# Performance work log

Hardware: AMD Instinct MI355X
Metric: run time of the kernel (lower is better)

## Reference

```python
import jax, jax.numpy as jnp
import numpy as np

NUM_HEADS = 12
HEAD_DIM = 128
DIM = NUM_HEADS * HEAD_DIM  # 1536
FRAMES = 8
GRID_H, GRID_W = 15, 26
SPATIAL = GRID_H * GRID_W  # 390
SEQ = FRAMES * SPATIAL      # 3120
EPS = 1e-5


def setup_inputs() -> dict:
    key = jax.random.key(0)
    ks = jax.random.split(key, 12)
    w = lambda k, shape, s=0.02: jax.random.normal(k, shape, dtype=jnp.float32) * s
    return {
        "x": jax.random.normal(ks[0], (1, SEQ, DIM), dtype=jnp.float32),
        "freqs": jax.random.uniform(ks[1], (SEQ, HEAD_DIM // 2), dtype=jnp.float32) * 6.283,
        "Wq": w(ks[2], (DIM, DIM)), "bq": jnp.zeros((DIM,), jnp.float32), "gq": jnp.ones((DIM,), jnp.float32),
        "Wk": w(ks[3], (DIM, DIM)), "bk": jnp.zeros((DIM,), jnp.float32), "gk": jnp.ones((DIM,), jnp.float32),
        "Wv": w(ks[4], (DIM, DIM)), "bv": jnp.zeros((DIM,), jnp.float32),
        "Wo": w(ks[5], (DIM, DIM)), "bo": jnp.zeros((DIM,), jnp.float32),
        "qk_frame_bias": w(ks[6], (FRAMES, DIM), 0.05),
        "v_frame_bias": w(ks[7], (FRAMES, DIM), 0.05),
        "v_spatial_bias": w(ks[8], (SPATIAL, DIM), 0.05),
    }


def _rmsnorm(x, g):
    return x * jax.lax.rsqrt(jnp.mean(x * x, axis=-1, keepdims=True) + EPS) * g


def _rope(x, freqs):
    # x: [b, s, dim] -> per-head interleaved complex rotation (Wan-style)
    b, s, _ = x.shape
    xp = x.reshape(b, s, NUM_HEADS, HEAD_DIM // 2, 2)
    cos = jnp.cos(freqs)[None, :, None, :]  # [1, s, 1, d/2]
    sin = jnp.sin(freqs)[None, :, None, :]
    xr, xi = xp[..., 0], xp[..., 1]
    out = jnp.stack([xr * cos - xi * sin, xr * sin + xi * cos], axis=-1)
    return out.reshape(b, s, DIM)


def _expand_frame(bias):
    # [FRAMES, dim] -> [1, FRAMES*SPATIAL, dim] (each frame vector repeated over spatial tokens)
    return jnp.broadcast_to(bias[:, None, :], (FRAMES, SPATIAL, DIM)).reshape(1, SEQ, DIM)


def _expand_spatial(bias):
    # [SPATIAL, dim] -> [1, FRAMES*SPATIAL, dim] (tiled over frames)
    return jnp.broadcast_to(bias[None, :, :], (FRAMES, SPATIAL, DIM)).reshape(1, SEQ, DIM)


def reference(x, freqs, Wq, bq, gq, Wk, bk, gk, Wv, bv, Wo, bo,
              qk_frame_bias, v_frame_bias, v_spatial_bias):
    q = _rmsnorm(x @ Wq + bq, gq)
    k = _rmsnorm(x @ Wk + bk, gk)
    v = x @ Wv + bv
    q = _rope(q, freqs)
    k = _rope(k, freqs)
    qk_bias = _expand_frame(qk_frame_bias)
    q = q + qk_bias
    k = k + qk_bias
    v = v + _expand_frame(v_frame_bias) + _expand_spatial(v_spatial_bias)
    b, s, _ = x.shape
    qh = q.reshape(b, s, NUM_HEADS, HEAD_DIM)
    kh = k.reshape(b, s, NUM_HEADS, HEAD_DIM)
    vh = v.reshape(b, s, NUM_HEADS, HEAD_DIM)
    scale = 1.0 / np.sqrt(HEAD_DIM)
    scores = jnp.einsum("bqnd,bknd->bnqk", qh, kh) * scale
    attn = jax.nn.softmax(scores, axis=-1)
    out = jnp.einsum("bnqk,bknd->bqnd", attn, vh).reshape(b, s, DIM)
    return out @ Wo + bo
```

## Files before the change

kernel.cpp:

```cpp
#include <hip/hip_runtime.h>
#include <cstdint>

#define SEQ     3120
#define SPAD    3200
#define DIM     1536
#define NQKV    4608
#define HEADS   12
#define HD      128
#define SPATIAL 390
#define EPSV    1e-5f
#define KVBLK   64
#define NTILES  49
#define NEGBIG  (-1e30f)
#define QSCALE  (0.08838834764831845f * 1.4426950408889634f)
#define CROW(r, hi) ((((r) & 3) + 8 * ((r) >> 2)) + 4 * (hi))

typedef unsigned short u16;
typedef short s16x8 __attribute__((ext_vector_type(8)));
typedef float f32x4 __attribute__((ext_vector_type(4)));
typedef float f32x16 __attribute__((ext_vector_type(16)));

__device__ __forceinline__ u16 f2bf(float f) {
  union { float f; unsigned u; } v; v.f = f;
  unsigned r = v.u + 0x7FFFu + ((v.u >> 16) & 1u);
  return (u16)(r >> 16);
}
__device__ __forceinline__ float bf2f(u16 b) {
  union { unsigned u; float f; } v; v.u = ((unsigned)b) << 16;
  return v.f;
}
__device__ __forceinline__ unsigned cvtpk(float lo, float hi) {
  unsigned r;
  asm("v_cvt_pk_bf16_f32 %0, %1, %2" : "=v"(r) : "v"(lo), "v"(hi));
  return r;
}
__device__ __forceinline__ void gload16(const void* g, const void* l) {
  __builtin_amdgcn_global_load_lds(
      (const __attribute__((address_space(1))) unsigned*)g,
      (__attribute__((address_space(3))) unsigned*)(uintptr_t)l,
      16, 0, 0);
}

__global__ __launch_bounds__(256) void k_convert_x(const float* __restrict__ x,
                                                   u16* __restrict__ xb) {
  const int i = (blockIdx.x * 256 + threadIdx.x) * 4;
  if (i >= SPAD * DIM) return;
  const int row = i / DIM;
  float4 v = make_float4(0.f, 0.f, 0.f, 0.f);
  if (row < SEQ) v = *(const float4*)(x + i);
  const unsigned lo = (unsigned)f2bf(v.x) | ((unsigned)f2bf(v.y) << 16);
  const unsigned hi = (unsigned)f2bf(v.z) | ((unsigned)f2bf(v.w) << 16);
  *(uint2*)(xb + i) = make_uint2(lo, hi);
}

__global__ __launch_bounds__(256) void k_transpose_w(
    const float* __restrict__ Wq, const float* __restrict__ Wk,
    const float* __restrict__ Wv, const float* __restrict__ Wo,
    u16* __restrict__ WtAll, u16* __restrict__ WoT) {
  const int wsel = blockIdx.z;
  const float* W = (wsel == 0) ? Wq : (wsel == 1) ? Wk : (wsel == 2) ? Wv : Wo;
  __shared__ float t[32][33];
  const int k0 = blockIdx.x * 32, n0 = blockIdx.y * 32;
  const int c = threadIdx.x & 31, r8 = threadIdx.x >> 5;
#pragma unroll
  for (int rr = 0; rr < 32; rr += 8)
    t[r8 + rr][c] = W[(size_t)(k0 + r8 + rr) * DIM + n0 + c];
  __syncthreads();
  u16* Wt = (wsel < 3) ? (WtAll + (size_t)wsel * DIM * DIM) : WoT;
#pragma unroll
  for (int rr = 0; rr < 32; rr += 8)
    Wt[(size_t)(n0 + r8 + rr) * DIM + k0 + c] = f2bf(t[c][r8 + rr]);
}

__global__ void k_biascat(const float* __restrict__ bq, const float* __restrict__ bk,
                          const float* __restrict__ bv, float* __restrict__ bcat) {
  const int i = blockIdx.x * 256 + threadIdx.x;
  if (i >= NQKV) return;
  bcat[i] = (i < DIM) ? bq[i] : (i < 2 * DIM) ? bk[i - DIM] : bv[i - 2 * DIM];
}

template <int OUT_BF16>
__global__ __launch_bounds__(256) void k_gemm(const u16* __restrict__ A,
                                              const u16* __restrict__ Bt,
                                              const float* __restrict__ bias,
                                              void* __restrict__ Cout,
                                              int N, int K, int storeMmax) {
  __shared__ short As[4096];
  __shared__ short Bs[4096];
  const int tid = threadIdx.x;
  const int lane = tid & 63, wv = tid >> 6;
  const int l15 = lane & 15, g = lane >> 4;
  const int brow = blockIdx.y * 128, bcol = blockIdx.x * 128;
  const int wr = wv >> 1, wc = wv & 1;

  const f32x4 z4 = {0.f, 0.f, 0.f, 0.f};
  f32x4 acc[4][4];
#pragma unroll
  for (int m = 0; m < 4; ++m)
#pragma unroll
    for (int n = 0; n < 4; ++n) acc[m][n] = z4;

  const int srow = wv * 16 + (lane >> 2);
  const int skk = (lane & 3) * 8;
  const u16* Ab = A + (size_t)(brow + srow) * K + skk;
  const u16* Bb = Bt + (size_t)(bcol + srow) * K + skk;
  short* AsW = As + wv * 512;
  short* BsW = Bs + wv * 512;
  const size_t step64 = (size_t)64 * K;

  for (int k0 = 0; k0 < K; k0 += 32) {
    __syncthreads();
    gload16(Ab + k0, AsW);
    gload16(Ab + k0 + step64, AsW + 2048);
    gload16(Bb + k0, BsW);
    gload16(Bb + k0 + step64, BsW + 2048);
    __syncthreads();
    s16x8 a[4], b[4];
#pragma unroll
    for (int m = 0; m < 4; ++m)
      a[m] = *(const s16x8*)&As[(wr * 64 + m * 16 + l15) * 32 + g * 8];
#pragma unroll
    for (int n = 0; n < 4; ++n)
      b[n] = *(const s16x8*)&Bs[(wc * 64 + n * 16 + l15) * 32 + g * 8];
#pragma unroll
    for (int m = 0; m < 4; ++m)
#pragma unroll
      for (int n = 0; n < 4; ++n)
        acc[m][n] = __builtin_amdgcn_mfma_f32_16x16x32_bf16(a[m], b[n], acc[m][n], 0, 0, 0);
  }

#pragma unroll
  for (int m = 0; m < 4; ++m) {
#pragma unroll
    for (int n = 0; n < 4; ++n) {
      const int cc = bcol + wc * 64 + n * 16 + l15;
      const float bb = bias[cc];
#pragma unroll
      for (int i = 0; i < 4; ++i) {
        const int r = brow + wr * 64 + m * 16 + g * 4 + i;
        if (r < storeMmax) {
          const float v = acc[m][n][i] + bb;
          if (OUT_BF16) ((u16*)Cout)[(size_t)r * N + cc] = f2bf(v);
          else          ((float*)Cout)[(size_t)r * N + cc] = v;
        }
      }
    }
  }
}

__global__ __launch_bounds__(256) void k_post(
    const u16* __restrict__ Pqkv, const float* __restrict__ freqs,
    const float* __restrict__ gq, const float* __restrict__ gk,
    const float* __restrict__ qkfb, const float* __restrict__ vfb,
    const float* __restrict__ vsb,
    u16* __restrict__ Qf, u16* __restrict__ Kf, u16* __restrict__ Vf) {
  const int s = blockIdx.x;
  const int t = threadIdx.x;
  const int fidx = s / SPATIAL;
  const int sp = s - fidx * SPATIAL;
  __shared__ float cs[64], sn[64];
  __shared__ float red[8];
  if (t < 64) {
    const float a = freqs[s * 64 + t];
    cs[t] = __cosf(a);
    sn[t] = __sinf(a);
  }
  const u16* qrow = Pqkv + (size_t)s * NQKV;
  const u16* krow = qrow + DIM;
  const u16* vrow = qrow + 2 * DIM;
  float sq = 0.f, sk = 0.f;
  for (int i = t; i < DIM; i += 256) {
    const float a = bf2f(qrow[i]); sq += a * a;
    const float b = bf2f(krow[i]); sk += b * b;
  }
#pragma unroll
  for (int off = 1; off < 64; off <<= 1) {
    sq += __shfl_xor(sq, off);
    sk += __shfl_xor(sk, off);
  }
  const int lane = t & 63, wv = t >> 6;
  if (lane == 0) { red[wv] = sq; red[wv + 4] = sk; }
  __syncthreads();
  sq = red[0] + red[1] + red[2] + red[3];
  sk = red[4] + red[5] + red[6] + red[7];
  const float rq = rsqrtf(sq * (1.0f / DIM) + EPSV);
  const float rk = rsqrtf(sk * (1.0f / DIM) + EPSV);
  for (int p = t; p < 768; p += 256) {
    const int d = 2 * p;
    const int pin = p & 63;
    const float c = cs[pin], s_ = sn[pin];
    const float bq0 = qkfb[fidx * DIM + d], bq1 = qkfb[fidx * DIM + d + 1];
    float xr = bf2f(qrow[d]) * rq * gq[d];
    float xi = bf2f(qrow[d + 1]) * rq * gq[d + 1];
    const float q0 = (xr * c - xi * s_ + bq0) * QSCALE;
    const float q1 = (xr * s_ + xi * c + bq1) * QSCALE;
    *(unsigned*)&Qf[(size_t)s * DIM + d] = (unsigned)f2bf(q0) | ((unsigned)f2bf(q1) << 16);
    xr = bf2f(krow[d]) * rk * gk[d];
    xi = bf2f(krow[d + 1]) * rk * gk[d + 1];
    const float k0 = xr * c - xi * s_ + bq0;
    const float k1 = xr * s_ + xi * c + bq1;
    *(unsigned*)&Kf[(size_t)s * DIM + d] = (unsigned)f2bf(k0) | ((unsigned)f2bf(k1) << 16);
    const float v0 = bf2f(vrow[d]) + vfb[fidx * DIM + d] + vsb[(size_t)sp * DIM + d];
    const float v1 = bf2f(vrow[d + 1]) + vfb[fidx * DIM + d + 1] + vsb[(size_t)sp * DIM + d + 1];
    *(unsigned*)&Vf[(size_t)s * DIM + d] = (unsigned)f2bf(v0) | ((unsigned)f2bf(v1) << 16);
  }
}

__global__ __launch_bounds__(256) void k_transpose_v(const u16* __restrict__ Vf,
                                                     u16* __restrict__ Vt) {
  __shared__ u16 tile[64][65];
  const int s0 = blockIdx.x * 64, c0 = blockIdx.y * 64;
  const int c = threadIdx.x & 63, r4 = threadIdx.x >> 6;
#pragma unroll
  for (int rr = 0; rr < 64; rr += 4) {
    const int s = s0 + r4 + rr;
    tile[r4 + rr][c] = (s < SEQ) ? Vf[(size_t)s * DIM + c0 + c] : (u16)0;
  }
  __syncthreads();
#pragma unroll
  for (int rr = 0; rr < 64; rr += 4) {
    const int dglob = c0 + r4 + rr;
    Vt[(size_t)dglob * SPAD + s0 + c] = tile[c][r4 + rr];
  }
}

__global__ __launch_bounds__(320, 2) void k_attn(const u16* __restrict__ Qf,
                                                 const u16* __restrict__ Kf,
                                                 const u16* __restrict__ Vt,
                                                 u16* __restrict__ AttO) {
  __shared__ short Ks[2][8192];
  __shared__ short Vs[2][8192];
  const int h = blockIdx.y;
  const int tid = threadIdx.x;
  const int lane = tid & 63, w = tid >> 6;
  const int l31 = lane & 31, hi = lane >> 5;
  const int qrow = blockIdx.x * 160 + w * 32 + l31;

  s16x8 qb[8];
  {
    const u16* qp = Qf + (size_t)qrow * DIM + h * HD + hi * 8;
#pragma unroll
    for (int s = 0; s < 8; ++s) qb[s] = *(const s16x8*)(qp + s * 16);
  }

  f32x16 o[4];
#pragma unroll
  for (int d = 0; d < 4; ++d)
#pragma unroll
    for (int r = 0; r < 16; ++r) o[d][r] = 0.f;
  float sl = 0.f;

  const u16* Kp[4];
  const u16* Vp[4];
  if (w < 4) {
#pragma unroll
    for (int it = 0; it < 4; ++it) {
      const int krow = w * 16 + it * 4 + (lane >> 4);
      const int kch = (lane & 15) ^ (it * 4 + (lane >> 4));
      Kp[it] = Kf + (size_t)krow * DIM + h * HD + kch * 8;
      const int vrow = w * 32 + it * 8 + (lane >> 3);
      const int vch = (lane & 7) ^ (lane >> 3);
      Vp[it] = Vt + (size_t)(h * HD + vrow) * SPAD + vch * 8;
    }
  }
  auto stage = [&](int T, int B) {
    const size_t kof = (size_t)T * KVBLK * DIM;
    const int vof = T * KVBLK;
#pragma unroll
    for (int it = 0; it < 4; ++it) {
      gload16(Kp[it] + kof, &Ks[B][(w * 16 + it * 4) * 128]);
      gload16(Vp[it] + vof, &Vs[B][(w * 32 + it * 8) * 64]);
    }
  };

  if (w < 4) {
    asm volatile("s_waitcnt vmcnt(0)" ::: "memory");
    stage(0, 0);
  }

  for (int t = 0; t < NTILES; ++t) {
    const int b = t & 1;
    if (w < 4) {
      if (t + 1 < NTILES) {
        stage(t + 1, b ^ 1);
        asm volatile("s_waitcnt vmcnt(8)" ::: "memory");
      } else {
        asm volatile("s_waitcnt vmcnt(0)" ::: "memory");
      }
    }
    __builtin_amdgcn_s_barrier();
    __builtin_amdgcn_sched_barrier(0);

    f32x16 st[2];
#pragma unroll
    for (int r = 0; r < 16; ++r) { st[0][r] = 0.f; st[1][r] = 0.f; }
    __builtin_amdgcn_s_setprio(1);
#pragma unroll
    for (int grp = 0; grp < 2; ++grp)
#pragma unroll
      for (int s = 0; s < 8; ++s) {
        const s16x8 ka = *(const s16x8*)&Ks[b][(grp * 32 + l31) * 128 +
                                              (((2 * s + hi) ^ (lane & 15)) * 8)];
        st[grp] = __builtin_amdgcn_mfma_f32_32x32x16_bf16(ka, qb[s], st[grp], 0, 0, 0);
      }
    __builtin_amdgcn_s_setprio(0);

    s16x8 vb[4][4];
#pragma unroll
    for (int s = 0; s < 4; ++s)
#pragma unroll
      for (int d = 0; d < 4; ++d)
        vb[s][d] = *(const s16x8*)&Vs[b][(d * 32 + l31) * 64 +
                                         (((2 * s + hi) ^ (lane & 7)) * 8)];

    if (t == NTILES - 1) {
#pragma unroll
      for (int r = 8; r < 16; ++r) st[1][r] = NEGBIG;
    }
    unsigned W[16], X[16];
    float p0s = 0.f, p1s = 0.f, p2s = 0.f, p3s = 0.f;
#pragma unroll
    for (int grp = 0; grp < 2; ++grp)
#pragma unroll
      for (int i = 0; i < 8; ++i) {
        const float p0 = exp2f(st[grp][2 * i]);
        const float p1 = exp2f(st[grp][2 * i + 1]);
        if (grp) { p2s += p0; p3s += p1; } else { p0s += p0; p1s += p1; }
        W[grp * 8 + i] = cvtpk(p0, p1);
      }
    sl += (p0s + p1s) + (p2s + p3s);
#pragma unroll
    for (int j = 0; j < 16; ++j) X[j] = __shfl_xor((int)W[j], 32);

    __builtin_amdgcn_s_setprio(1);
#pragma unroll
    for (int s = 0; s < 4; ++s) {
      const int base = (s >> 1) * 8 + (s & 1) * 4;
      unsigned pw[4];
      pw[0] = hi ? X[base + 2] : W[base + 0];
      pw[1] = hi ? X[base + 3] : W[base + 1];
      pw[2] = hi ? W[base + 2] : X[base + 0];
      pw[3] = hi ? W[base + 3] : X[base + 1];
      const s16x8 pa = *(const s16x8*)pw;
#pragma unroll
      for (int d = 0; d < 4; ++d)
        o[d] = __builtin_amdgcn_mfma_f32_32x32x16_bf16(pa, vb[s][d], o[d], 0, 0, 0);
    }
    __builtin_amdgcn_s_setprio(0);
    __builtin_amdgcn_s_barrier();
    __builtin_amdgcn_sched_barrier(0);
  }

  sl += __shfl_xor(sl, 32);
  const float rs = 1.0f / sl;
#pragma unroll
  for (int r = 0; r < 16; ++r) {
    const float rq = __shfl(rs, CROW(r, hi));
    const int row = blockIdx.x * 160 + w * 32 + CROW(r, hi);
    if (row < SEQ) {
#pragma unroll
      for (int d = 0; d < 4; ++d)
        AttO[(size_t)row * DIM + h * HD + d * 32 + l31] = f2bf(o[d][r] * rq);
    }
  }
}

extern "C" void kernel_launch(void* const* d_in, const int* in_sizes, int n_in,
                              void* d_out, int out_size, void* d_ws, size_t ws_size,
                              hipStream_t stream) {
  const float* x    = (const float*)d_in[0];
  const float* freqs= (const float*)d_in[1];
  const float* Wq   = (const float*)d_in[2];
  const float* bq   = (const float*)d_in[3];
  const float* gq   = (const float*)d_in[4];
  const float* Wk   = (const float*)d_in[5];
  const float* bk   = (const float*)d_in[6];
  const float* gk   = (const float*)d_in[7];
  const float* Wv   = (const float*)d_in[8];
  const float* bv   = (const float*)d_in[9];
  const float* Wo   = (const float*)d_in[10];
  const float* bo   = (const float*)d_in[11];
  const float* qkfb = (const float*)d_in[12];
  const float* vfb  = (const float*)d_in[13];
  const float* vsb  = (const float*)d_in[14];

  if (ws_size < (size_t)87705600) return;

  char* ws = (char*)d_ws;
  u16*   xb    = (u16*)(ws);
  u16*   Vt    = (u16*)(ws);
  u16*   WtAll = (u16*)(ws + 9830400);
  u16*   WoT   = (u16*)(ws + 23986176);
  float* bcat  = (float*)(ws + 28704768);
  u16*   Pqkv  = (u16*)(ws + 28723200);
  u16*   AttO  = (u16*)(ws + 28723200);
  u16*   Qf    = (u16*)(ws + 58214400);
  u16*   Kf    = (u16*)(ws + 68044800);
  u16*   Vf    = (u16*)(ws + 77875200);

  k_convert_x<<<4800, 256, 0, stream>>>(x, xb);
  k_transpose_w<<<dim3(48, 48, 4), 256, 0, stream>>>(Wq, Wk, Wv, Wo, WtAll, WoT);
  k_biascat<<<18, 256, 0, stream>>>(bq, bk, bv, bcat);
  k_gemm<1><<<dim3(36, 25), 256, 0, stream>>>(xb, WtAll, bcat, Pqkv, NQKV, DIM, SPAD);
  k_post<<<SEQ, 256, 0, stream>>>(Pqkv, freqs, gq, gk, qkfb, vfb, vsb, Qf, Kf, Vf);
  k_transpose_v<<<dim3(50, 24), 256, 0, stream>>>(Vf, Vt);
  k_attn<<<dim3(20, 12), 320, 0, stream>>>(Qf, Kf, Vt, AttO);
  k_gemm<0><<<dim3(12, 25), 256, 0, stream>>>(AttO, WoT, bo, d_out, DIM, DIM, SEQ);
}
```

Before: 282.9 us.

## Shrink attention blocks to 64 queries with 32-key tiles and fold bias concat

Attention blocks now hold 2 waves (64 query rows) instead of 5 waves (160 rows), and all waves load K/V. The KV tile shrinks from 64 to 32 keys, with 98 iterations and smaller LDS buffers and swizzles adjusted to match. The grid grows from 240 to 600 blocks, which should fill the 256 CUs more evenly than 240 blocks did. The cost is that each block reloads the full K/V per 64 queries, so K/V traffic rises, and barriers per unit of work increase. The separate bias-concatenation kernel is merged into the x conversion kernel to save one launch.

Result: slower. 296.8 us (+4.9%).

```diff
diff --git a/kernel.cpp b/kernel.cpp
--- a/kernel.cpp
+++ b/kernel.cpp
@@ -9,8 +9,8 @@
 #define HD      128
 #define SPATIAL 390
 #define EPSV    1e-5f
-#define KVBLK   64
-#define NTILES  49
+#define AKV     32
+#define ANT     98
 #define NEGBIG  (-1e30f)
 #define QSCALE  (0.08838834764831845f * 1.4426950408889634f)
 #define CROW(r, hi) ((((r) & 3) + 8 * ((r) >> 2)) + 4 * (hi))
@@ -41,8 +41,14 @@
       16, 0, 0);
 }
 
-__global__ __launch_bounds__(256) void k_convert_x(const float* __restrict__ x,
-                                                   u16* __restrict__ xb) {
+__global__ __launch_bounds__(256) void k_convert_x(
+    const float* __restrict__ x, const float* __restrict__ bq,
+    const float* __restrict__ bk, const float* __restrict__ bv,
+    u16* __restrict__ xb, float* __restrict__ bcat) {
+  if (blockIdx.x == 0) {
+    for (int j = threadIdx.x; j < NQKV; j += 256)
+      bcat[j] = (j < DIM) ? bq[j] : (j < 2 * DIM) ? bk[j - DIM] : bv[j - 2 * DIM];
+  }
   const int i = (blockIdx.x * 256 + threadIdx.x) * 4;
   if (i >= SPAD * DIM) return;
   const int row = i / DIM;
@@ -70,13 +76,6 @@
 #pragma unroll
   for (int rr = 0; rr < 32; rr += 8)
     Wt[(size_t)(n0 + r8 + rr) * DIM + k0 + c] = f2bf(t[c][r8 + rr]);
-}
-
-__global__ void k_biascat(const float* __restrict__ bq, const float* __restrict__ bk,
-                          const float* __restrict__ bv, float* __restrict__ bcat) {
-  const int i = blockIdx.x * 256 + threadIdx.x;
-  if (i >= NQKV) return;
-  bcat[i] = (i < DIM) ? bq[i] : (i < 2 * DIM) ? bk[i - DIM] : bv[i - 2 * DIM];
 }
 
 template <int OUT_BF16>
@@ -224,17 +223,17 @@
   }
 }
 
-__global__ __launch_bounds__(320, 2) void k_attn(const u16* __restrict__ Qf,
+__global__ __launch_bounds__(128, 2) void k_attn(const u16* __restrict__ Qf,
                                                  const u16* __restrict__ Kf,
                                                  const u16* __restrict__ Vt,
                                                  u16* __restrict__ AttO) {
-  __shared__ short Ks[2][8192];
-  __shared__ short Vs[2][8192];
+  __shared__ short Ks[2][4096];
+  __shared__ short Vs[2][4096];
   const int h = blockIdx.y;
   const int tid = threadIdx.x;
   const int lane = tid & 63, w = tid >> 6;
   const int l31 = lane & 31, hi = lane >> 5;
-  const int qrow = blockIdx.x * 160 + w * 32 + l31;
+  const int qrow = blockIdx.x * 64 + w * 32 + l31;
 
   s16x8 qb[8];
   {
@@ -252,95 +251,84 @@
 
   const u16* Kp[4];
   const u16* Vp[4];
-  if (w < 4) {
-#pragma unroll
-    for (int it = 0; it < 4; ++it) {
-      const int krow = w * 16 + it * 4 + (lane >> 4);
-      const int kch = (lane & 15) ^ (it * 4 + (lane >> 4));
-      Kp[it] = Kf + (size_t)krow * DIM + h * HD + kch * 8;
-      const int vrow = w * 32 + it * 8 + (lane >> 3);
-      const int vch = (lane & 7) ^ (lane >> 3);
-      Vp[it] = Vt + (size_t)(h * HD + vrow) * SPAD + vch * 8;
-    }
+#pragma unroll
+  for (int it = 0; it < 4; ++it) {
+    const int krow = w * 16 + it * 4 + (lane >> 4);
+    const int kch = (lane & 15) ^ (it * 4 + (lane >> 4));
+    Kp[it] = Kf + (size_t)krow * DIM + h * HD + kch * 8;
+    const int vrow = w * 64 + it * 16 + (lane >> 2);
+    const int vch = (lane & 3) ^ ((lane >> 2) & 3);
+    Vp[it] = Vt + (size_t)(h * HD + vrow) * SPAD + vch * 8;
   }
   auto stage = [&](int T, int B) {
-    const size_t kof = (size_t)T * KVBLK * DIM;
-    const int vof = T * KVBLK;
+    const size_t kof = (size_t)T * AKV * DIM;
+    const int vof = T * AKV;
 #pragma unroll
     for (int it = 0; it < 4; ++it) {
       gload16(Kp[it] + kof, &Ks[B][(w * 16 + it * 4) * 128]);
-      gload16(Vp[it] + vof, &Vs[B][(w * 32 + it * 8) * 64]);
+      gload16(Vp[it] + vof, &Vs[B][(w * 64 + it * 16) * 32]);
     }
   };
 
-  if (w < 4) {
-    asm volatile("s_waitcnt vmcnt(0)" ::: "memory");
-    stage(0, 0);
-  }
-
-  for (int t = 0; t < NTILES; ++t) {
+  asm volatile("s_waitcnt vmcnt(0)" ::: "memory");
+  stage(0, 0);
+
+  for (int t = 0; t < ANT; ++t) {
     const int b = t & 1;
-    if (w < 4) {
-      if (t + 1 < NTILES) {
-        stage(t + 1, b ^ 1);
-        asm volatile("s_waitcnt vmcnt(8)" ::: "memory");
-      } else {
-        asm volatile("s_waitcnt vmcnt(0)" ::: "memory");
-      }
+    if (t + 1 < ANT) {
+      stage(t + 1, b ^ 1);
+      asm volatile("s_waitcnt vmcnt(8)" ::: "memory");
+    } else {
+      asm volatile("s_waitcnt vmcnt(0)" ::: "memory");
     }
     __builtin_amdgcn_s_barrier();
     __builtin_amdgcn_sched_barrier(0);
 
-    f32x16 st[2];
-#pragma unroll
-    for (int r = 0; r < 16; ++r) { st[0][r] = 0.f; st[1][r] = 0.f; }
+    f32x16 st;
+#pragma unroll
+    for (int r = 0; r < 16; ++r) st[r] = 0.f;
     __builtin_amdgcn_s_setprio(1);
 #pragma unroll
-    for (int grp = 0; grp < 2; ++grp)
-#pragma unroll
-      for (int s = 0; s < 8; ++s) {
-        const s16x8 ka = *(const s16x8*)&Ks[b][(grp * 32 + l31) * 128 +
-                                              (((2 * s + hi) ^ (lane & 15)) * 8)];
-        st[grp] = __builtin_amdgcn_mfma_f32_32x32x16_bf16(ka, qb[s], st[grp], 0, 0, 0);
-      }
+    for (int s = 0; s < 8; ++s) {
+      const s16x8 ka = *(const s16x8*)&Ks[b][l31 * 128 +
+                                            (((2 * s + hi) ^ (l31 & 15)) * 8)];
+      st = __builtin_amdgcn_mfma_f32_32x32x16_bf16(ka, qb[s], st, 0, 0, 0);
+    }
     __builtin_amdgcn_s_setprio(0);
 
-    s16x8 vb[4][4];
-#pragma unroll
-    for (int s = 0; s < 4; ++s)
+    s16x8 vb[2][4];
+#pragma unroll
+    for (int s = 0; s < 2; ++s)
 #pragma unroll
       for (int d = 0; d < 4; ++d)
-        vb[s][d] = *(const s16x8*)&Vs[b][(d * 32 + l31) * 64 +
-                                         (((2 * s + hi) ^ (lane & 7)) * 8)];
-
-    if (t == NTILES - 1) {
-#pragma unroll
-      for (int r = 8; r < 16; ++r) st[1][r] = NEGBIG;
-    }
-    unsigned W[16], X[16];
-    float p0s = 0.f, p1s = 0.f, p2s = 0.f, p3s = 0.f;
-#pragma unroll
-    for (int grp = 0; grp < 2; ++grp)
-#pragma unroll
-      for (int i = 0; i < 8; ++i) {
-        const float p0 = exp2f(st[grp][2 * i]);
-        const float p1 = exp2f(st[grp][2 * i + 1]);
-        if (grp) { p2s += p0; p3s += p1; } else { p0s += p0; p1s += p1; }
-        W[grp * 8 + i] = cvtpk(p0, p1);
-      }
-    sl += (p0s + p1s) + (p2s + p3s);
-#pragma unroll
-    for (int j = 0; j < 16; ++j) X[j] = __shfl_xor((int)W[j], 32);
+        vb[s][d] = *(const s16x8*)&Vs[b][(d * 32 + l31) * 32 +
+                                         (((2 * s + hi) ^ (l31 & 3)) * 8)];
+
+    if (t == ANT - 1) {
+#pragma unroll
+      for (int r = 8; r < 16; ++r) st[r] = NEGBIG;
+    }
+    unsigned W[8], X[8];
+    float p0s = 0.f, p1s = 0.f;
+#pragma unroll
+    for (int i = 0; i < 8; ++i) {
+      const float p0 = exp2f(st[2 * i]);
+      const float p1 = exp2f(st[2 * i + 1]);
+      p0s += p0; p1s += p1;
+      W[i] = cvtpk(p0, p1);
+    }
+    sl += p0s + p1s;
+#pragma unroll
+    for (int j = 0; j < 8; ++j) X[j] = __shfl_xor((int)W[j], 32);
 
     __builtin_amdgcn_s_setprio(1);
 #pragma unroll
-    for (int s = 0; s < 4; ++s) {
-      const int base = (s >> 1) * 8 + (s & 1) * 4;
+    for (int s = 0; s < 2; ++s) {
       unsigned pw[4];
-      pw[0] = hi ? X[base + 2] : W[base + 0];
-      pw[1] = hi ? X[base + 3] : W[base + 1];
-      pw[2] = hi ? W[base + 2] : X[base + 0];
-      pw[3] = hi ? W[base + 3] : X[base + 1];
+      pw[0] = hi ? X[s * 4 + 2] : W[s * 4 + 0];
+      pw[1] = hi ? X[s * 4 + 3] : W[s * 4 + 1];
+      pw[2] = hi ? W[s * 4 + 2] : X[s * 4 + 0];
+      pw[3] = hi ? W[s * 4 + 3] : X[s * 4 + 1];
       const s16x8 pa = *(const s16x8*)pw;
 #pragma unroll
       for (int d = 0; d < 4; ++d)
@@ -356,7 +344,7 @@
 #pragma unroll
   for (int r = 0; r < 16; ++r) {
     const float rq = __shfl(rs, CROW(r, hi));
-    const int row = blockIdx.x * 160 + w * 32 + CROW(r, hi);
+    const int row = blockIdx.x * 64 + w * 32 + CROW(r, hi);
     if (row < SEQ) {
 #pragma unroll
       for (int d = 0; d < 4; ++d)
@@ -398,12 +386,11 @@
   u16*   Kf    = (u16*)(ws + 68044800);
   u16*   Vf    = (u16*)(ws + 77875200);
 
-  k_convert_x<<<4800, 256, 0, stream>>>(x, xb);
+  k_convert_x<<<4800, 256, 0, stream>>>(x, bq, bk, bv, xb, bcat);
   k_transpose_w<<<dim3(48, 48, 4), 256, 0, stream>>>(Wq, Wk, Wv, Wo, WtAll, WoT);
-  k_biascat<<<18, 256, 0, stream>>>(bq, bk, bv, bcat);
   k_gemm<1><<<dim3(36, 25), 256, 0, stream>>>(xb, WtAll, bcat, Pqkv, NQKV, DIM, SPAD);
   k_post<<<SEQ, 256, 0, stream>>>(Pqkv, freqs, gq, gk, qkfb, vfb, vsb, Qf, Kf, Vf);
   k_transpose_v<<<dim3(50, 24), 256, 0, stream>>>(Vf, Vt);
-  k_attn<<<dim3(20, 12), 320, 0, stream>>>(Qf, Kf, Vt, AttO);
+  k_attn<<<dim3(50, 12), 128, 0, stream>>>(Qf, Kf, Vt, AttO);
   k_gemm<0><<<dim3(12, 25), 256, 0, stream>>>(AttO, WoT, bo, d_out, DIM, DIM, SEQ);
 }
```

## Widen GEMM K-step to 64 with XOR-swizzled LDS and XCD-aware block mapping

Applied to the files above, without the earlier changes.

The GEMM now stages 64-wide K slices per iteration, which halves the number of barrier pairs. It uses an XOR swizzle on the LDS column chunks to avoid bank conflicts on the fragment reads. A 1D grid with an XCD-aware remap groups neighbouring tiles on the same chiplet to improve L2 reuse. The bias-concatenation kernel is folded into the x-conversion kernel, removing one launch. LDS use per block doubles, which may reduce occupancy.

Measured after the change: 259.5 us. 8.3% less time.

```diff
diff --git a/kernel.cpp b/kernel.cpp
--- a/kernel.cpp
+++ b/kernel.cpp
@@ -41,8 +41,14 @@
       16, 0, 0);
 }
 
-__global__ __launch_bounds__(256) void k_convert_x(const float* __restrict__ x,
-                                                   u16* __restrict__ xb) {
+__global__ __launch_bounds__(256) void k_convert_x(
+    const float* __restrict__ x, const float* __restrict__ bq,
+    const float* __restrict__ bk, const float* __restrict__ bv,
+    u16* __restrict__ xb, float* __restrict__ bcat) {
+  if (blockIdx.x == 0) {
+    for (int j = threadIdx.x; j < NQKV; j += 256)
+      bcat[j] = (j < DIM) ? bq[j] : (j < 2 * DIM) ? bk[j - DIM] : bv[j - 2 * DIM];
+  }
   const int i = (blockIdx.x * 256 + threadIdx.x) * 4;
   if (i >= SPAD * DIM) return;
   const int row = i / DIM;
@@ -72,25 +78,25 @@
     Wt[(size_t)(n0 + r8 + rr) * DIM + k0 + c] = f2bf(t[c][r8 + rr]);
 }
 
-__global__ void k_biascat(const float* __restrict__ bq, const float* __restrict__ bk,
-                          const float* __restrict__ bv, float* __restrict__ bcat) {
-  const int i = blockIdx.x * 256 + threadIdx.x;
-  if (i >= NQKV) return;
-  bcat[i] = (i < DIM) ? bq[i] : (i < 2 * DIM) ? bk[i - DIM] : bv[i - 2 * DIM];
-}
-
 template <int OUT_BF16>
 __global__ __launch_bounds__(256) void k_gemm(const u16* __restrict__ A,
                                               const u16* __restrict__ Bt,
                                               const float* __restrict__ bias,
                                               void* __restrict__ Cout,
-                                              int N, int K, int storeMmax) {
-  __shared__ short As[4096];
-  __shared__ short Bs[4096];
+                                              int N, int K, int storeMmax,
+                                              int nbx) {
+  __shared__ short As[8192];
+  __shared__ short Bs[8192];
+  const int nwg = gridDim.x;
+  const int q = nwg >> 3, r = nwg & 7;
+  const int xcd = blockIdx.x & 7, idx = blockIdx.x >> 3;
+  const int swz = (xcd < r ? xcd * (q + 1) : r * (q + 1) + (xcd - r) * q) + idx;
+  const int bxi = swz % nbx, byi = swz / nbx;
+  const int brow = byi * 128, bcol = bxi * 128;
+
   const int tid = threadIdx.x;
   const int lane = tid & 63, wv = tid >> 6;
   const int l15 = lane & 15, g = lane >> 4;
-  const int brow = blockIdx.y * 128, bcol = blockIdx.x * 128;
   const int wr = wv >> 1, wc = wv & 1;
 
   const f32x4 z4 = {0.f, 0.f, 0.f, 0.f};
@@ -100,33 +106,41 @@
 #pragma unroll
     for (int n = 0; n < 4; ++n) acc[m][n] = z4;
 
-  const int srow = wv * 16 + (lane >> 2);
-  const int skk = (lane & 3) * 8;
-  const u16* Ab = A + (size_t)(brow + srow) * K + skk;
-  const u16* Bb = Bt + (size_t)(bcol + srow) * K + skk;
-  short* AsW = As + wv * 512;
-  short* BsW = Bs + wv * 512;
-  const size_t step64 = (size_t)64 * K;
-
-  for (int k0 = 0; k0 < K; k0 += 32) {
+  const u16* Ap[4];
+  const u16* Bp[4];
+  const int sch = ((lane & 7) ^ ((lane >> 3) & 7)) * 8;
+#pragma unroll
+  for (int it = 0; it < 4; ++it) {
+    const int row = it * 32 + wv * 8 + (lane >> 3);
+    Ap[it] = A + (size_t)(brow + row) * K + sch;
+    Bp[it] = Bt + (size_t)(bcol + row) * K + sch;
+  }
+
+  for (int k0 = 0; k0 < K; k0 += 64) {
     __syncthreads();
-    gload16(Ab + k0, AsW);
-    gload16(Ab + k0 + step64, AsW + 2048);
-    gload16(Bb + k0, BsW);
-    gload16(Bb + k0 + step64, BsW + 2048);
+#pragma unroll
+    for (int it = 0; it < 4; ++it) {
+      gload16(Ap[it] + k0, As + (it * 32 + wv * 8) * 64);
+      gload16(Bp[it] + k0, Bs + (it * 32 + wv * 8) * 64);
+    }
     __syncthreads();
-    s16x8 a[4], b[4];
-#pragma unroll
-    for (int m = 0; m < 4; ++m)
-      a[m] = *(const s16x8*)&As[(wr * 64 + m * 16 + l15) * 32 + g * 8];
-#pragma unroll
-    for (int n = 0; n < 4; ++n)
-      b[n] = *(const s16x8*)&Bs[(wc * 64 + n * 16 + l15) * 32 + g * 8];
-#pragma unroll
-    for (int m = 0; m < 4; ++m)
+#pragma unroll
+    for (int kk = 0; kk < 2; ++kk) {
+      s16x8 a[4], b[4];
+#pragma unroll
+      for (int m = 0; m < 4; ++m)
+        a[m] = *(const s16x8*)&As[(wr * 64 + m * 16 + l15) * 64 +
+                                  (((kk * 4 + g) ^ (l15 & 7)) * 8)];
 #pragma unroll
       for (int n = 0; n < 4; ++n)
-        acc[m][n] = __builtin_amdgcn_mfma_f32_16x16x32_bf16(a[m], b[n], acc[m][n], 0, 0, 0);
+        b[n] = *(const s16x8*)&Bs[(wc * 64 + n * 16 + l15) * 64 +
+                                  (((kk * 4 + g) ^ (l15 & 7)) * 8)];
+#pragma unroll
+      for (int m = 0; m < 4; ++m)
+#pragma unroll
+        for (int n = 0; n < 4; ++n)
+          acc[m][n] = __builtin_amdgcn_mfma_f32_16x16x32_bf16(a[m], b[n], acc[m][n], 0, 0, 0);
+    }
   }
 
 #pragma unroll
@@ -137,11 +151,11 @@
       const float bb = bias[cc];
 #pragma unroll
       for (int i = 0; i < 4; ++i) {
-        const int r = brow + wr * 64 + m * 16 + g * 4 + i;
-        if (r < storeMmax) {
+        const int rr = brow + wr * 64 + m * 16 + g * 4 + i;
+        if (rr < storeMmax) {
           const float v = acc[m][n][i] + bb;
-          if (OUT_BF16) ((u16*)Cout)[(size_t)r * N + cc] = f2bf(v);
-          else          ((float*)Cout)[(size_t)r * N + cc] = v;
+          if (OUT_BF16) ((u16*)Cout)[(size_t)rr * N + cc] = f2bf(v);
+          else          ((float*)Cout)[(size_t)rr * N + cc] = v;
         }
       }
     }
@@ -398,12 +412,11 @@
   u16*   Kf    = (u16*)(ws + 68044800);
   u16*   Vf    = (u16*)(ws + 77875200);
 
-  k_convert_x<<<4800, 256, 0, stream>>>(x, xb);
+  k_convert_x<<<4800, 256, 0, stream>>>(x, bq, bk, bv, xb, bcat);
   k_transpose_w<<<dim3(48, 48, 4), 256, 0, stream>>>(Wq, Wk, Wv, Wo, WtAll, WoT);
-  k_biascat<<<18, 256, 0, stream>>>(bq, bk, bv, bcat);
-  k_gemm<1><<<dim3(36, 25), 256, 0, stream>>>(xb, WtAll, bcat, Pqkv, NQKV, DIM, SPAD);
+  k_gemm<1><<<900, 256, 0, stream>>>(xb, WtAll, bcat, Pqkv, NQKV, DIM, SPAD, 36);
   k_post<<<SEQ, 256, 0, stream>>>(Pqkv, freqs, gq, gk, qkfb, vfb, vsb, Qf, Kf, Vf);
   k_transpose_v<<<dim3(50, 24), 256, 0, stream>>>(Vf, Vt);
   k_attn<<<dim3(20, 12), 320, 0, stream>>>(Qf, Kf, Vt, AttO);
-  k_gemm<0><<<dim3(12, 25), 256, 0, stream>>>(AttO, WoT, bo, d_out, DIM, DIM, SEQ);
-}
+  k_gemm<0><<<300, 256, 0, stream>>>(AttO, WoT, bo, d_out, DIM, DIM, SEQ, 12);
+}
```
